# Performance work log

Hardware: AMD Instinct MI355X
Metric: run time of the kernel (lower is better)

The kernel has to match this reference:

```python
import jax, jax.numpy as jnp
import numpy as np
import math

B = 128      # bandwidth
BATCH = 2048 # flat batch (samples x channels)


def _dlt_weights(Bv):
    # Driscoll-Healy quadrature weights, length 2B
    k = np.arange(2 * Bv)
    p = np.arange(Bv)
    C = 2.0 / Bv * np.sin(np.pi * (2 * k + 1) / (4.0 * Bv))
    S = np.sin(np.outer(2 * k + 1, 2 * p + 1) * np.pi / (4.0 * Bv))  # [2B,B]
    return C * (S @ (1.0 / (2 * p + 1)))


def _idct_matrix(N):
    k = np.arange(N)[:, None]
    n = np.arange(N)[None, :]
    DI = np.cos(np.pi * n * (k + 0.5) / N)
    DI[:, 0] *= np.sqrt(1.0 / N)
    DI[:, 1:] *= np.sqrt(2.0 / N)
    return DI


def _idst_matrix(N):
    k = np.arange(N)[:, None]
    n = np.arange(N)[None, :]
    DI = np.sin(np.pi * (n + 1) * (k + 0.5) / N)
    DI[:, N - 1] = (-1.0) ** np.arange(N)
    DI[:, :N - 1] *= np.sqrt(2.0 / N)
    DI[:, N - 1] *= np.sqrt(1.0 / N)
    return DI


def _little_half(Bv):
    # Wigner little-d at beta=pi/2 via 3-term recurrence (vectorized over m,n)
    Bm1 = Bv - 1
    s2 = np.sqrt(2.0)
    d = np.zeros((Bv, 2 * Bv - 1, 2 * Bv - 1))
    d[0, Bm1, Bm1] = 1.0
    d[1, Bm1 - 1, Bm1 - 1] = 0.5
    d[1, Bm1 - 1, Bm1] = 1.0 / s2
    d[1, Bm1 - 1, Bm1 + 1] = 0.5
    d[1, Bm1, Bm1 - 1] = -1.0 / s2
    d[1, Bm1, Bm1 + 1] = 1.0 / s2
    d[1, Bm1 + 1, Bm1 - 1] = 0.5
    d[1, Bm1 + 1, Bm1] = -1.0 / s2
    d[1, Bm1 + 1, Bm1 + 1] = 0.5
    for l in range(2, Bv):
        m = np.arange(l).astype(np.float64)
        M, Nn = np.meshgrid(m, m, indexing='ij')
        denom = (l - 1.0) * np.sqrt((l - M) * (l + M) * (l - Nn) * (l + Nn))
        c1 = (1.0 - 2.0 * l) * M * Nn / denom
        c2 = -l * np.sqrt(((l - 1.0) ** 2 - M ** 2) * ((l - 1.0) ** 2 - Nn ** 2)) / denom
        d[l, Bm1:Bm1 + l, Bm1:Bm1 + l] = (c1 * d[l - 1, Bm1:Bm1 + l, Bm1:Bm1 + l]
                                          + c2 * d[l - 2, Bm1:Bm1 + l, Bm1:Bm1 + l])
        mm = np.arange(l + 1)
        lnV = np.array([0.5 * (math.lgamma(2 * l + 1) - math.lgamma(l + mi + 1)
                               - math.lgamma(l - mi + 1)) - l * math.log(2.0) for mi in mm])
        v = np.exp(lnV)
        d[l, Bm1 + mm, Bm1 + l] = v
        d[l, Bm1 + l, Bm1 + mm] = ((-1.0) ** (l - mm)) * v
        # symmetry fill (write order a1, a2, a3 reproduces torch loop semantics)
        sub = d[l, Bm1:Bm1 + l + 1, Bm1:Bm1 + l + 1].copy()
        M2, N2 = np.meshgrid(np.arange(l + 1), np.arange(l + 1), indexing='ij')
        a1 = ((-1.0) ** (M2 - N2)) * sub
        a2 = ((-1.0) ** (l - N2)) * sub
        a3 = ((-1.0) ** (l + M2)) * sub
        a1[0, 0] = sub[0, 0]
        a2[0, 0] = sub[0, 0]
        a3[0, 0] = sub[0, 0]
        d[l, Bm1 - l:Bm1 + 1, Bm1 - l:Bm1 + 1] = a1[::-1, ::-1]
        d[l, Bm1 - l:Bm1 + 1, Bm1:Bm1 + l + 1] = a2[::-1, :]
        d[l, Bm1:Bm1 + l + 1, Bm1 - l:Bm1 + 1] = a3[:, ::-1]
    return d


def _wigner_coeffs(Bv, d):
    Bm1 = Bv - 1
    N = 2 * Bv
    D = np.zeros((Bv, Bv, N))
    for m in range(Bv):
        for l in range(m, Bv):
            if m % 2 == 0:
                n = np.arange(l + 1)
                c = np.sqrt((2 * l + 1) / 2.0) * np.where(n == 0, np.sqrt(N), np.sqrt(2.0 * N))
                if m % 4 == 2:
                    c = -c
                coeff = c * d[l, n + Bm1, Bm1 - m] * d[l, n + Bm1, Bm1]
                coeff = np.where(np.abs(coeff) > 1e-15, coeff, 0.0)
                D[m, l, :l + 1] = coeff
            else:
                n = np.arange(l)  # n == l gives 0
                if l > 0:
                    c = np.sqrt((2 * l + 1) / 2.0) * np.sqrt(2.0 * N)
                    if m % 4 == 1:
                        c = -c
                    coeff = c * d[l, n + 1 + Bm1, Bm1 - m] * d[l, n + 1 + Bm1, Bm1]
                    coeff = np.where(np.abs(coeff) > 1e-15, coeff, 0.0)
                    D[m, l, :l] = coeff
    return D


def _buffers(Bv):
    N = 2 * Bv
    Wd = np.diag(_dlt_weights(Bv))
    XFc = Wd @ _idct_matrix(N)   # weighted DCT matrix (applied as x @ XFc)
    XFs = Wd @ _idst_matrix(N)   # weighted DST matrix
    D = _wigner_coeffs(Bv, _little_half(Bv))
    cm = ((-1.0) ** (Bv - 1)) * np.sqrt(1.0 / (2.0 * np.pi))  # Cm[B-1] scalar
    return XFc, XFs, D, cm


def setup_inputs() -> dict:
    key = jax.random.key(0)
    psiHat = jax.random.normal(key, (BATCH, B, 2 * B), dtype=jnp.float32)
    XFc, XFs, D, cm = _buffers(B)
    return {
        'psiHat': psiHat,
        'cm': jnp.float32(cm),
        'XFc': jnp.asarray(XFc, dtype=jnp.float32),
        'XFs': jnp.asarray(XFs, dtype=jnp.float32),
        'D': jnp.asarray(D, dtype=jnp.float32),
    }


def reference(psiHat, cm, XFc, XFs, D):
    # psiHat: [batch, B, 2B]; XFc/XFs: [2B, 2B]; D: [B, B, 2B]
    psi = psiHat * cm  # Cm[B-1:] broadcasts as a scalar
    # F.linear with weight = XF.T  ==  x @ XF on the last axis
    psi = psi.at[:, 0::2, :].set(jnp.einsum('bmi,ij->bmj', psi[:, 0::2, :], XFc))
    psi = psi.at[:, 1::2, :].set(jnp.einsum('bmi,ij->bmj', psi[:, 1::2, :], XFs))
    # per-order-m block matmul against Wigner coefficient blocks
    return jnp.einsum('bmi,moi->bmo', psi, D)
```

## Files before the change

### kernel.cpp

```cpp
#include <hip/hip_runtime.h>


typedef __attribute__((ext_vector_type(8))) short short8;
typedef __attribute__((ext_vector_type(4))) float f32x4;

#define NBATCH 2048
#define NM 128
#define NI 256
#define NO 128
#define BPACK_M 32768

#define NSLAB 8
#define SLABROWS 16
#define LDSBUF 16384

#define GLB(p) ((const __attribute__((address_space(1))) void*)(p))
#define LDS(p) ((__attribute__((address_space(3))) void*)(p))

__device__ __forceinline__ unsigned short f2bf(float f) {
  unsigned int u = __builtin_bit_cast(unsigned int, f);
  u += 0x7FFFu + ((u >> 16) & 1u);
  return (unsigned short)(u >> 16);
}

__device__ __forceinline__ short8 cvt8(float4 a, float4 b, float s) {
  short8 v;
  v[0] = (short)f2bf(s * a.x); v[1] = (short)f2bf(s * a.y);
  v[2] = (short)f2bf(s * a.z); v[3] = (short)f2bf(s * a.w);
  v[4] = (short)f2bf(s * b.x); v[5] = (short)f2bf(s * b.y);
  v[6] = (short)f2bf(s * b.z); v[7] = (short)f2bf(s * b.w);
  return v;
}

__global__ __launch_bounds__(256) void e_kernel(
    const float* __restrict__ XFc, const float* __restrict__ XFs,
    const float* __restrict__ D, const float* __restrict__ cmp,
    unsigned short* __restrict__ Bpack)
{
  const int m = blockIdx.x >> 1;
  const int ihalf = blockIdx.x & 1;
  const int tid = threadIdx.x;
  const int lane = tid & 63;
  const int w = tid >> 6;
  const int lr = lane & 15;
  const int lg = lane >> 4;
  const float cm = cmp[0];
  const float* __restrict__ Xp = (m & 1) ? XFs : XFc;
  const float* __restrict__ Dm = D + (size_t)m * (NO * NI);
  const int i0 = ihalf * 128 + w * 32;

  f32x4 acc[2][8];
#pragma unroll
  for (int a = 0; a < 2; a++)
#pragma unroll
    for (int b = 0; b < 8; b++) acc[a][b] = (f32x4)0.f;

  for (int kk = 0; kk < NI; kk += 32) {
    const int kb = kk + lg * 8;
    short8 af[2];
#pragma unroll
    for (int rf = 0; rf < 2; rf++) {
      const float* ap = Xp + (size_t)(i0 + rf * 16 + lr) * NI + kb;
      float4 x0 = *(const float4*)ap;
      float4 x1 = *(const float4*)(ap + 4);
      af[rf] = cvt8(x0, x1, cm);
    }
    short8 bf[8];
#pragma unroll
    for (int cf = 0; cf < 8; cf++) {
      const float* bp = Dm + (size_t)(cf * 16 + lr) * NI + kb;
      float4 x0 = *(const float4*)bp;
      float4 x1 = *(const float4*)(bp + 4);
      bf[cf] = cvt8(x0, x1, 1.0f);
    }
#pragma unroll
    for (int rf = 0; rf < 2; rf++)
#pragma unroll
      for (int cf = 0; cf < 8; cf++)
        acc[rf][cf] = __builtin_amdgcn_mfma_f32_16x16x32_bf16(
            af[rf], bf[cf], acc[rf][cf], 0, 0, 0);
  }

  unsigned short* Bm = Bpack + (size_t)m * BPACK_M;
#pragma unroll
  for (int rf = 0; rf < 2; rf++) {
    const int t = (i0 + rf * 16) >> 5;
    const int L = ((2 * rf + (lg >> 1)) & 3) * 16 + lr;
#pragma unroll
    for (int cf = 0; cf < 8; cf++) {
      ushort4 pk;
      pk.x = f2bf(acc[rf][cf][0]);
      pk.y = f2bf(acc[rf][cf][1]);
      pk.z = f2bf(acc[rf][cf][2]);
      pk.w = f2bf(acc[rf][cf][3]);
      *(ushort4*)(Bm + (size_t)(t * 8 + cf) * 512 + L * 8 + (lg & 1) * 4) = pk;
    }
  }
}

#define SB __builtin_amdgcn_sched_barrier(0)

__global__ __launch_bounds__(256, 4) void fdlt_main(
    const float* __restrict__ psiHat,
    const unsigned short* __restrict__ Bpack,
    float* __restrict__ out)
{
  __shared__ float As_f[2 * SLABROWS * 256];
  const int m = blockIdx.x;
  const int tid = threadIdx.x;
  const int lane = tid & 63;
  const int w = tid >> 6;
  const int bbase = blockIdx.y * (NSLAB * SLABROWS);
  const int lr = lane & 15;
  const int lg = lane >> 4;
  const int cfbase = w * 2;
  char* As = (char*)As_f;

  const unsigned short* __restrict__ Bm = Bpack + (size_t)m * BPACK_M;

  short8 ball[8][2];
#pragma unroll
  for (int t = 0; t < 8; t++)
#pragma unroll
    for (int j = 0; j < 2; j++)
      ball[t][j] = *(const short8*)(
          Bm + (size_t)(t * 8 + cfbase + j) * 512 + lane * 8);

  auto STAGE = [&](int s) {
#pragma unroll
    for (int j = 0; j < 4; j++) {
      const int r = j * 4 + w;
      const int fofs = ((lane ^ (r & 15)) << 2);
      const float* src =
          psiHat + ((size_t)(bbase + s * SLABROWS + r) * NM + m) * NI + fofs;
      __builtin_amdgcn_global_load_lds(GLB(src),
                                       LDS(As + (s & 1) * LDSBUF + r * 1024),
                                       16, 0, 0);
    }
  };

  f32x4 acc[2];

  STAGE(0);
  STAGE(1);
  asm volatile("s_waitcnt vmcnt(4)" ::: "memory");
  SB;
  __builtin_amdgcn_s_barrier();
  SB;

  for (int s = 0; s < NSLAB; s++) {
    const char* Arow = As + (s & 1) * LDSBUF + lr * 1024;
#pragma unroll
    for (int j = 0; j < 2; j++) acc[j] = (f32x4)0.f;
#pragma unroll
    for (int t = 0; t < 8; t++) {
      const int p0 = ((((t * 4 + lg) << 1) ^ lr) << 4);
      float4 x0 = *(const float4*)(Arow + p0);
      float4 x1 = *(const float4*)(Arow + (p0 ^ 16));
      short8 af = cvt8(x0, x1, 1.0f);
#pragma unroll
      for (int j = 0; j < 2; j++)
        acc[j] = __builtin_amdgcn_mfma_f32_16x16x32_bf16(
            af, ball[t][j], acc[j], 0, 0, 0);
    }

#pragma unroll
    for (int j = 0; j < 2; j++) {
      const int o = (cfbase + j) * 16 + lr;
#pragma unroll
      for (int r = 0; r < 4; r++) {
        const int b = bbase + s * SLABROWS + lg * 4 + r;
        out[((size_t)b * NM + m) * NO + o] = acc[j][r];
      }
    }
    SB;

    if (s + 1 < NSLAB) {
      __builtin_amdgcn_s_barrier();
      SB;
      if (s + 2 < NSLAB) {
        STAGE(s + 2);
        asm volatile("s_waitcnt vmcnt(12)" ::: "memory");
      } else {
        asm volatile("s_waitcnt vmcnt(8)" ::: "memory");
      }
      SB;
      __builtin_amdgcn_s_barrier();
      SB;
    }
  }
}

extern "C" void kernel_launch(void* const* d_in, const int* in_sizes, int n_in,
                              void* d_out, int out_size, void* d_ws, size_t ws_size,
                              hipStream_t stream) {
  const float* psiHat = (const float*)d_in[0];
  const float* cm     = (const float*)d_in[1];
  const float* XFc    = (const float*)d_in[2];
  const float* XFs    = (const float*)d_in[3];
  const float* D      = (const float*)d_in[4];
  float* out = (float*)d_out;
  unsigned short* Bpack = (unsigned short*)d_ws;

  e_kernel<<<256, 256, 0, stream>>>(XFc, XFs, D, cm, Bpack);
  fdlt_main<<<dim3(NM, NBATCH / (NSLAB * SLABROWS)), 256, 0, stream>>>(
      psiHat, Bpack, out);
}
```

Before: 106.7 us.

## Stage psiHat through registers instead of direct global-to-LDS loads

Replaces the direct global_load_lds staging of psiHat slabs with ordinary float4 register loads that are later written to LDS, using two register buffers and a fully unrolled slab loop. The load for slab s+2 is issued at the start of slab s's compute, and the register-to-LDS write for the next slab happens after the stores, removing one barrier per iteration. This costs extra VGPRs (32 floats of staging), which may reduce occupancy at 4 waves/SIMD. It also depends on hand-tuned vmcnt counts that must match the compiler's ordering of loads and stores.

```diff
diff --git a/kernel.cpp b/kernel.cpp
--- a/kernel.cpp
+++ b/kernel.cpp
@@ -13,9 +13,6 @@
 #define NSLAB 8
 #define SLABROWS 16
 #define LDSBUF 16384
-
-#define GLB(p) ((const __attribute__((address_space(1))) void*)(p))
-#define LDS(p) ((__attribute__((address_space(3))) void*)(p))
 
 __device__ __forceinline__ unsigned short f2bf(float f) {
   unsigned int u = __builtin_bit_cast(unsigned int, f);
@@ -126,29 +123,40 @@
       ball[t][j] = *(const short8*)(
           Bm + (size_t)(t * 8 + cfbase + j) * 512 + lane * 8);
 
-  auto STAGE = [&](int s) {
+  float4 xaA[4], xaB[4];
+  auto LOADR = [&](int s, float4* xa) {
 #pragma unroll
     for (int j = 0; j < 4; j++) {
       const int r = j * 4 + w;
       const int fofs = ((lane ^ (r & 15)) << 2);
-      const float* src =
-          psiHat + ((size_t)(bbase + s * SLABROWS + r) * NM + m) * NI + fofs;
-      __builtin_amdgcn_global_load_lds(GLB(src),
-                                       LDS(As + (s & 1) * LDSBUF + r * 1024),
-                                       16, 0, 0);
+      xa[j] = *(const float4*)(
+          psiHat + ((size_t)(bbase + s * SLABROWS + r) * NM + m) * NI + fofs);
     }
   };
+  auto WRITELDS = [&](int s, const float4* xa) {
+#pragma unroll
+    for (int j = 0; j < 4; j++) {
+      const int r = j * 4 + w;
+      *(float4*)(As + (s & 1) * LDSBUF + r * 1024 + lane * 16) = xa[j];
+    }
+  };
 
   f32x4 acc[2];
 
-  STAGE(0);
-  STAGE(1);
+  LOADR(0, xaA);
+  LOADR(1, xaB);
   asm volatile("s_waitcnt vmcnt(4)" ::: "memory");
+  SB;
+  WRITELDS(0, xaA);
+  asm volatile("s_waitcnt lgkmcnt(0)" ::: "memory");
   SB;
   __builtin_amdgcn_s_barrier();
   SB;
 
+#pragma unroll
   for (int s = 0; s < NSLAB; s++) {
+    if (s + 2 < NSLAB) LOADR(s + 2, (s & 1) ? xaB : xaA);
+
     const char* Arow = As + (s & 1) * LDSBUF + lr * 1024;
 #pragma unroll
     for (int j = 0; j < 2; j++) acc[j] = (f32x4)0.f;
@@ -176,14 +184,15 @@
     SB;
 
     if (s + 1 < NSLAB) {
-      __builtin_amdgcn_s_barrier();
+      if (s == 0)
+        asm volatile("s_waitcnt vmcnt(12)" ::: "memory");
+      else if (s + 2 < NSLAB)
+        asm volatile("s_waitcnt vmcnt(20)" ::: "memory");
+      else
+        asm volatile("s_waitcnt vmcnt(16)" ::: "memory");
       SB;
-      if (s + 2 < NSLAB) {
-        STAGE(s + 2);
-        asm volatile("s_waitcnt vmcnt(12)" ::: "memory");
-      } else {
-        asm volatile("s_waitcnt vmcnt(8)" ::: "memory");
-      }
+      WRITELDS(s + 1, (s & 1) ? xaA : xaB);
+      asm volatile("s_waitcnt lgkmcnt(0)" ::: "memory");
       SB;
       __builtin_amdgcn_s_barrier();
       SB;
```

New measurement: 245.5 us. 130% more time.

## Process two adjacent orders per block with doubled LDS staging

Applied to the files above, without the earlier changes.

Each block of the main kernel now handles two consecutive orders m. Each wave owns one order and four output column fragments, and the LDS slab buffers are doubled to hold both orders' rows, so each batch row loads a contiguous 2 KB span. The grid is halved and launch bounds drop to two blocks per SM. This trades fewer, larger blocks and more B-fragment registers for better-coalesced global reads, with some risk to latency hiding.

```diff
diff --git a/kernel.cpp b/kernel.cpp
--- a/kernel.cpp
+++ b/kernel.cpp
@@ -12,7 +12,7 @@
 
 #define NSLAB 8
 #define SLABROWS 16
-#define LDSBUF 16384
+#define ABUF 32768
 
 #define GLB(p) ((const __attribute__((address_space(1))) void*)(p))
 #define LDS(p) ((__attribute__((address_space(3))) void*)(p))
@@ -100,58 +100,62 @@
 
 #define SB __builtin_amdgcn_sched_barrier(0)
 
-__global__ __launch_bounds__(256, 4) void fdlt_main(
+__global__ __launch_bounds__(256, 2) void fdlt_main(
     const float* __restrict__ psiHat,
     const unsigned short* __restrict__ Bpack,
     float* __restrict__ out)
 {
-  __shared__ float As_f[2 * SLABROWS * 256];
-  const int m = blockIdx.x;
+  __shared__ float As_f[2 * SLABROWS * 2 * 256];
+  const int m0 = blockIdx.x * 2;
   const int tid = threadIdx.x;
   const int lane = tid & 63;
   const int w = tid >> 6;
   const int bbase = blockIdx.y * (NSLAB * SLABROWS);
   const int lr = lane & 15;
   const int lg = lane >> 4;
-  const int cfbase = w * 2;
+  const int mm = w & 1;
+  const int oh = w >> 1;
+  const int mw = m0 + mm;
   char* As = (char*)As_f;
 
-  const unsigned short* __restrict__ Bm = Bpack + (size_t)m * BPACK_M;
-
-  short8 ball[8][2];
+  const unsigned short* __restrict__ Bm = Bpack + (size_t)mw * BPACK_M;
+  short8 ball[8][4];
 #pragma unroll
   for (int t = 0; t < 8; t++)
 #pragma unroll
-    for (int j = 0; j < 2; j++)
+    for (int j = 0; j < 4; j++)
       ball[t][j] = *(const short8*)(
-          Bm + (size_t)(t * 8 + cfbase + j) * 512 + lane * 8);
+          Bm + (size_t)(t * 8 + oh * 4 + j) * 512 + lane * 8);
 
   auto STAGE = [&](int s) {
 #pragma unroll
     for (int j = 0; j < 4; j++) {
       const int r = j * 4 + w;
       const int fofs = ((lane ^ (r & 15)) << 2);
-      const float* src =
-          psiHat + ((size_t)(bbase + s * SLABROWS + r) * NM + m) * NI + fofs;
-      __builtin_amdgcn_global_load_lds(GLB(src),
-                                       LDS(As + (s & 1) * LDSBUF + r * 1024),
-                                       16, 0, 0);
+      const float* src0 =
+          psiHat + ((size_t)(bbase + s * SLABROWS + r) * NM + m0) * NI;
+#pragma unroll
+      for (int h = 0; h < 2; h++) {
+        __builtin_amdgcn_global_load_lds(
+            GLB(src0 + h * NI + fofs),
+            LDS(As + (s & 1) * ABUF + (r * 2 + h) * 1024), 16, 0, 0);
+      }
     }
   };
 
-  f32x4 acc[2];
+  f32x4 acc[4];
 
   STAGE(0);
   STAGE(1);
-  asm volatile("s_waitcnt vmcnt(4)" ::: "memory");
+  asm volatile("s_waitcnt vmcnt(8)" ::: "memory");
   SB;
   __builtin_amdgcn_s_barrier();
   SB;
 
   for (int s = 0; s < NSLAB; s++) {
-    const char* Arow = As + (s & 1) * LDSBUF + lr * 1024;
-#pragma unroll
-    for (int j = 0; j < 2; j++) acc[j] = (f32x4)0.f;
+    const char* Arow = As + (s & 1) * ABUF + (lr * 2 + mm) * 1024;
+#pragma unroll
+    for (int j = 0; j < 4; j++) acc[j] = (f32x4)0.f;
 #pragma unroll
     for (int t = 0; t < 8; t++) {
       const int p0 = ((((t * 4 + lg) << 1) ^ lr) << 4);
@@ -159,18 +163,18 @@
       float4 x1 = *(const float4*)(Arow + (p0 ^ 16));
       short8 af = cvt8(x0, x1, 1.0f);
 #pragma unroll
-      for (int j = 0; j < 2; j++)
+      for (int j = 0; j < 4; j++)
         acc[j] = __builtin_amdgcn_mfma_f32_16x16x32_bf16(
             af, ball[t][j], acc[j], 0, 0, 0);
     }
 
 #pragma unroll
-    for (int j = 0; j < 2; j++) {
-      const int o = (cfbase + j) * 16 + lr;
+    for (int j = 0; j < 4; j++) {
+      const int o = (oh * 4 + j) * 16 + lr;
 #pragma unroll
       for (int r = 0; r < 4; r++) {
         const int b = bbase + s * SLABROWS + lg * 4 + r;
-        out[((size_t)b * NM + m) * NO + o] = acc[j][r];
+        out[((size_t)b * NM + mw) * NO + o] = acc[j][r];
       }
     }
     SB;
@@ -180,9 +184,9 @@
       SB;
       if (s + 2 < NSLAB) {
         STAGE(s + 2);
-        asm volatile("s_waitcnt vmcnt(12)" ::: "memory");
+        asm volatile("s_waitcnt vmcnt(24)" ::: "memory");
       } else {
-        asm volatile("s_waitcnt vmcnt(8)" ::: "memory");
+        asm volatile("s_waitcnt vmcnt(16)" ::: "memory");
       }
       SB;
       __builtin_amdgcn_s_barrier();
@@ -203,6 +207,6 @@
   unsigned short* Bpack = (unsigned short*)d_ws;
 
   e_kernel<<<256, 256, 0, stream>>>(XFc, XFs, D, cm, Bpack);
-  fdlt_main<<<dim3(NM, NBATCH / (NSLAB * SLABROWS)), 256, 0, stream>>>(
+  fdlt_main<<<dim3(NM / 2, NBATCH / (NSLAB * SLABROWS)), 256, 0, stream>>>(
       psiHat, Bpack, out);
 }
```

New measurement: 113.4 us. 1.06x slower.
